# Kernel tuning notes

Hardware: AMD Instinct MI355X
Metric: run time of the kernel (lower is better)

## Reference

```python
import jax, jax.numpy as jnp
import numpy as np
import math

# Dims: d_model=192, expand=2 -> d_inner=d_ssm=384, headdim=64 -> nheads=6,
# d_state=128, K=4 scan directions, ngroups=1 (directions fused into state dim).
D_MODEL = 192
D_STATE = 128
D_CONV = 3
EXPAND = 2
HEADDIM = 64
CHUNK = 256
D_INNER = EXPAND * D_MODEL          # 384
D_SSM = D_INNER                     # default d_ssm (d_mlp == 0)
NHEADS = D_SSM // HEADDIM           # 6
K = 4                               # scan directions
HTOT = K * NHEADS                   # 24 heads in the fused scan
NSTATE = K * D_STATE                # 512 fused state dim (ngroups=1)
CONV_BC = 2 * D_STATE + NHEADS      # 262
B, H, W = 2, 64, 64


def _dwconv(x, w, b):
    # x: (B,C,H,W), w: (C,1,k,k) depthwise, SAME padding ((k-1)//2)
    y = jax.lax.conv_general_dilated(
        x, w, (1, 1), [(1, 1), (1, 1)],
        feature_group_count=x.shape[1],
        dimension_numbers=('NCHW', 'OIHW', 'NCHW'))
    return y + b[None, :, None, None]


def _ssd(x, dt_raw, A_logs, Bm, Cm, Ds, dt_bias):
    # Mamba2 chunked selective scan (dt_softplus=True, default dt_limit).
    # x: (b,l,h,p)  dt_raw: (b,l,h)  Bm,Cm: (b,l,n) with ngroups=1
    A = -jnp.exp(A_logs)                              # (h,)
    dt = jax.nn.softplus(dt_raw + dt_bias)            # (b,l,h)
    b, l, h, p = x.shape
    n = Bm.shape[-1]
    nc = l // CHUNK
    xc = x.reshape(b, nc, CHUNK, h, p)
    dtc = dt.reshape(b, nc, CHUNK, h)
    Bc = Bm.reshape(b, nc, CHUNK, n)
    Cc = Cm.reshape(b, nc, CHUNK, n)
    dA = dtc * A                                      # (b,nc,cs,h)
    acum = jnp.cumsum(dA, axis=2)
    # intra-chunk (causal, attention-like)
    a_t = jnp.transpose(acum, (0, 1, 3, 2))           # (b,nc,h,cs)
    diff = a_t[..., :, None] - a_t[..., None, :]      # (b,nc,h,i,j)
    causal = jnp.tril(jnp.ones((CHUNK, CHUNK), bool))
    Lmat = jnp.where(causal, jnp.exp(diff), 0.0)
    CB = jnp.einsum('bcin,bcjn->bcij', Cc, Bc)        # (b,nc,i,j)
    M = CB[:, :, None] * Lmat * jnp.transpose(dtc, (0, 1, 3, 2))[:, :, :, None, :]
    y = jnp.einsum('bchij,bcjhp->bcihp', M, xc)
    # chunk-final states
    decay_end = jnp.exp(acum[:, :, -1:, :] - acum)    # (b,nc,cs,h)
    states = jnp.einsum('bcjh,bcjn,bcjhp->bchpn', decay_end * dtc, Bc, xc)
    chunk_decay = jnp.exp(acum[:, :, -1, :])          # (b,nc,h)

    def step(S, inp):
        st, dec = inp
        return S * dec[:, :, None, None] + st, S

    S0 = jnp.zeros((b, h, p, n), x.dtype)
    _, prev = jax.lax.scan(step, S0, (jnp.moveaxis(states, 1, 0),
                                      jnp.moveaxis(chunk_decay, 1, 0)))
    prev = jnp.moveaxis(prev, 0, 1)                   # (b,nc,h,p,n)
    y = y + jnp.einsum('bcih,bcin,bchpn->bcihp', jnp.exp(acum), Cc, prev)
    y = y + xc * Ds[:, None]                          # D skip connection
    return y.reshape(b, l, h, p)


def _branch(u, u_cross, W_skip, W_xs, W_bcdt, conv_xs_w, conv_xs_b,
            conv_bc_w, conv_bc_b, dt_bias, A_logs, Ds, norm_w, W_out):
    Bb, Hh, Ww, _ = u.shape
    L = Hh * Ww
    z = (u @ W_skip).reshape(Bb, L, D_SSM)            # gate (d_mlp == 0)
    xs = jnp.transpose(u @ W_xs, (0, 3, 1, 2))        # (B,d_ssm,H,W)
    xs = jax.nn.silu(_dwconv(xs, conv_xs_w, conv_xs_b))
    bc = jnp.transpose(u_cross @ W_bcdt, (0, 3, 1, 2))
    bc = jax.nn.silu(_dwconv(bc, conv_bc_w, conv_bc_b))
    xbc = jnp.concatenate([xs, bc], axis=1)           # (B,646,H,W)
    C = xbc.shape[1]
    v = xbc.reshape(Bb, C, L)                         # HW raster
    vt = jnp.transpose(xbc, (0, 1, 3, 2)).reshape(Bb, C, L)  # WH raster
    hw = jnp.stack([v, vt], axis=1)                   # (B,2,C,L)
    xbcdt = jnp.concatenate([hw, jnp.flip(hw, axis=-1)], axis=1)  # (B,4,C,L)
    xp = xbcdt[:, :, :D_SSM]
    Bp = xbcdt[:, :, D_SSM:D_SSM + D_STATE]
    Cp = xbcdt[:, :, D_SSM + D_STATE:D_SSM + 2 * D_STATE]
    dtp = xbcdt[:, :, D_SSM + 2 * D_STATE:]
    x = xp.reshape(Bb, K * D_SSM, L).transpose(0, 2, 1).reshape(Bb, L, HTOT, HEADDIM)
    Bm = Bp.reshape(Bb, NSTATE, L).transpose(0, 2, 1)
    Cm = Cp.reshape(Bb, NSTATE, L).transpose(0, 2, 1)
    dt = dtp.reshape(Bb, HTOT, L).transpose(0, 2, 1)
    y = _ssd(x, dt, A_logs, Bm, Cm, Ds, dt_bias)      # (B,L,24,64)
    y = y.reshape(Bb, L, K, D_SSM)
    out_y = y[:, :, 0]
    inv_y = jnp.flip(y[:, :, 2:4], axis=1)            # (B,L,2,d_ssm)
    wh_y = y[:, :, 1].reshape(Bb, Ww, Hh, D_SSM).transpose(0, 2, 1, 3).reshape(Bb, L, D_SSM)
    invwh_y = inv_y[:, :, 1].reshape(Bb, Ww, Hh, D_SSM).transpose(0, 2, 1, 3).reshape(Bb, L, D_SSM)
    yf = out_y + inv_y[:, :, 0] + wh_y + invwh_y
    # gated RMSNorm (norm_before_gate=False, group_size == d_ssm)
    g = yf * jax.nn.silu(z)
    g = g * jax.lax.rsqrt(jnp.mean(g * g, axis=-1, keepdims=True) + 1e-5) * norm_w
    return (g @ W_out).reshape(Bb, Hh, Ww, D_MODEL)


def setup_inputs():
    key = jax.random.key(0)
    ks = jax.random.split(key, 16)
    f = lambda i, s: jax.random.normal(ks[i], s, jnp.float32)
    sc = 0.02
    dt = jnp.exp(jax.random.uniform(ks[10], (NHEADS,)) *
                 (math.log(0.1) - math.log(0.001)) + math.log(0.001))
    dt = jnp.maximum(dt, 1e-4)
    inv_dt = dt + jnp.log(-jnp.expm1(-dt))
    A = jax.random.uniform(ks[11], (NHEADS,), minval=1.0, maxval=16.0)
    return {
        'u1': f(0, (B, H, W, D_MODEL)),
        'u2': f(1, (B, H, W, D_MODEL)),
        'u2_cat_u1': f(2, (B, H, W, D_MODEL)),
        'u1_cat_u2': f(3, (B, H, W, D_MODEL)),
        'W_skip': f(4, (D_MODEL, D_SSM)) * sc,
        'W_xs': f(5, (D_MODEL, D_SSM)) * sc,
        'W_bcdt': f(6, (D_MODEL, CONV_BC)) * sc,
        'conv_xs_w': f(7, (D_SSM, 1, D_CONV, D_CONV)) * sc,
        'conv_xs_b': jnp.zeros((D_SSM,), jnp.float32),
        'conv_bc_w': f(8, (CONV_BC, 1, D_CONV, D_CONV)) * sc,
        'conv_bc_b': jnp.zeros((CONV_BC,), jnp.float32),
        'dt_bias': jnp.tile(inv_dt, K),
        'A_logs': jnp.tile(jnp.log(A), K),
        'Ds': jnp.ones((HTOT,), jnp.float32),
        'norm_w': jnp.ones((D_SSM,), jnp.float32),
        'W_out': f(9, (D_SSM, D_MODEL)) * sc,
    }


def reference(u1, u2, u2_cat_u1, u1_cat_u2, W_skip, W_xs, W_bcdt,
              conv_xs_w, conv_xs_b, conv_bc_w, conv_bc_b,
              dt_bias, A_logs, Ds, norm_w, W_out):
    args = (W_skip, W_xs, W_bcdt, conv_xs_w, conv_xs_b, conv_bc_w,
            conv_bc_b, dt_bias, A_logs, Ds, norm_w, W_out)
    out1 = _branch(u1, u2_cat_u1, *args)
    out2 = _branch(u2, u1_cat_u2, *args)
    return out1, out2
```

## Files before the change

kernel.cpp:

```cpp
#include <hip/hip_runtime.h>
#include <hip/hip_bf16.h>

#define DEV __device__ __forceinline__

static constexpr int LL   = 4096;
static constexpr int GG   = 4;
static constexpr int CBC  = 262;

typedef float f32x4  __attribute__((ext_vector_type(4)));
typedef short bf16x8 __attribute__((ext_vector_type(8)));
typedef short bf16x4v __attribute__((ext_vector_type(4)));
typedef short bf16x2 __attribute__((ext_vector_type(2)));

DEV int map_l(int s, int k) {
    int m = (k & 2) ? (4095 - s) : s;
    if (k & 1) m = ((m & 63) << 6) | (m >> 6);
    return m;
}
DEV float silu_f(float x) { return x / (1.f + __expf(-x)); }
DEV short f2bf(float f) {
    union { __hip_bfloat16 h; short s; } u;
    u.h = __float2bfloat16(f);
    return u.s;
}
DEV float bf2f(short s) {
    return __uint_as_float(((unsigned)(unsigned short)s) << 16);
}
DEV bf16x8 pack8(float4 a, float4 b) {
    bf16x8 r;
    r[0]=f2bf(a.x); r[1]=f2bf(a.y); r[2]=f2bf(a.z); r[3]=f2bf(a.w);
    r[4]=f2bf(b.x); r[5]=f2bf(b.y); r[6]=f2bf(b.z); r[7]=f2bf(b.w);
    return r;
}
DEV bf16x8 load8u(const __hip_bfloat16* p) {
    bf16x4v lo = *(const bf16x4v*)p;
    bf16x4v hi = *(const bf16x4v*)(p + 4);
    bf16x8 r;
    r[0]=lo[0]; r[1]=lo[1]; r[2]=lo[2]; r[3]=lo[3];
    r[4]=hi[0]; r[5]=hi[1]; r[6]=hi[2]; r[7]=hi[3];
    return r;
}
DEV void store16(__hip_bfloat16* p, const float* v) {
    bf16x8 a, b;
    #pragma unroll
    for (int e = 0; e < 8; ++e) { a[e] = f2bf(v[e]); b[e] = f2bf(v[8+e]); }
    *(bf16x8*)p = a;
    *((bf16x8*)p + 1) = b;
}
DEV void storeT(float v, float* p) { *p = v; }
DEV void storeT(float v, __hip_bfloat16* p) { *p = __float2bfloat16(v); }

__global__ void sentinel_k(float* out) { out[0] = 1e30f; }

__global__ void wt_all_k(const float* __restrict__ W_skip, const float* __restrict__ W_xs,
                         const float* __restrict__ W_bcdt, const float* __restrict__ W_out,
                         const float* __restrict__ norm_w, __hip_bfloat16* __restrict__ Wt)
{
    int idx = blockIdx.x * 256 + threadIdx.x;
    if (idx < 73728) {
        int n = idx / 192, k = idx - n * 192;
        Wt[idx] = __float2bfloat16(W_skip[(size_t)k * 384 + n]);
    } else if (idx < 147456) {
        int r = idx - 73728;
        int n = r / 192, k = r - n * 192;
        Wt[idx] = __float2bfloat16(W_xs[(size_t)k * 384 + n]);
    } else if (idx < 208896) {
        int r = idx - 147456;
        int n = r / 192, k = r - n * 192;
        Wt[idx] = __float2bfloat16(n < 262 ? W_bcdt[(size_t)k * 262 + n] : 0.f);
    } else if (idx < 282624) {
        int r = idx - 208896;
        int n = r / 384, k = r - n * 384;
        Wt[idx] = __float2bfloat16(W_out[(size_t)k * 192 + n] * norm_w[k]);
    }
}

template<int MODE, typename AT, typename OutT>
DEV void mgemm_body(const AT* __restrict__ A0, const AT* __restrict__ A1,
                    const __hip_bfloat16* __restrict__ Wt, OutT* __restrict__ C,
                    OutT* __restrict__ C2, int N, int Kd, int i0, int j0)
{
    int t = threadIdx.x;
    int w = t >> 6, lane = t & 63;
    int lr = lane & 15, kq = lane >> 4;
    const AT* arow[2];
    #pragma unroll
    for (int a = 0; a < 2; ++a) {
        int grow = i0 + w * 32 + a * 16 + lr;
        const AT* Ap = (grow < 8192) ? A0 : A1;
        arow[a] = Ap + (size_t)(grow & 8191) * Kd;
    }
    f32x4 acc[2][4] = {};
    for (int k0 = 0; k0 < Kd; k0 += 32) {
        int kb = k0 + kq * 8;
        bf16x8 af[2];
        #pragma unroll
        for (int a = 0; a < 2; ++a) {
            if constexpr (sizeof(AT) == 4)
                af[a] = pack8(*(const float4*)(arow[a] + kb), *(const float4*)(arow[a] + kb + 4));
            else
                af[a] = *(const bf16x8*)(arow[a] + kb);
        }
        #pragma unroll
        for (int b = 0; b < 4; ++b) {
            int n = j0 + b * 16 + lr;
            bf16x8 bfr = *(const bf16x8*)(Wt + (size_t)n * Kd + kb);
            #pragma unroll
            for (int a = 0; a < 2; ++a)
                acc[a][b] = __builtin_amdgcn_mfma_f32_16x16x32_bf16(af[a], bfr, acc[a][b], 0, 0, 0);
        }
    }
    #pragma unroll
    for (int a = 0; a < 2; ++a)
        #pragma unroll
        for (int b = 0; b < 4; ++b)
            #pragma unroll
            for (int r = 0; r < 4; ++r) {
                int row = i0 + w * 32 + a * 16 + kq * 4 + r;
                int col = j0 + b * 16 + lr;
                float v = acc[a][b][r];
                if constexpr (MODE == 0) {
                    if (col < N) storeT(v, &C[(size_t)row * N + col]);
                } else if constexpr (MODE == 1) {
                    if (col < N) storeT(silu_f(v), &C[(size_t)row * N + col]);
                } else {
                    if (col < 384) storeT(silu_f(v), &C[(size_t)row * 384 + col]);
                    else           storeT(v, &C2[(size_t)row * 384 + col - 384]);
                }
            }
}

template<int MODE, typename AT, typename OutT>
__global__ __launch_bounds__(256) void mgemm_k(
    const AT* __restrict__ A0, const AT* __restrict__ A1,
    const __hip_bfloat16* __restrict__ Wt, OutT* __restrict__ C,
    OutT* __restrict__ C2, int N, int Kd)
{
    mgemm_body<MODE, AT, OutT>(A0, A1, Wt, C, C2, N, Kd,
                               blockIdx.y * 128, blockIdx.x * 64);
}

__global__ __launch_bounds__(256) void mgemm_in_k(
    const float* __restrict__ u1, const float* __restrict__ u2,
    const float* __restrict__ u21, const float* __restrict__ u12,
    const __hip_bfloat16* __restrict__ Wt_skip, const __hip_bfloat16* __restrict__ Wt_bcdt,
    __hip_bfloat16* __restrict__ z_silu, __hip_bfloat16* __restrict__ pre_xs,
    __hip_bfloat16* __restrict__ pre_bc)
{
    int bid = blockIdx.x;
    if (bid < 1536) {
        mgemm_body<2, float, __hip_bfloat16>(u1, u2, Wt_skip, z_silu, pre_xs,
                                             768, 192, (bid / 12) * 128, (bid % 12) * 64);
    } else {
        int b = bid - 1536;
        mgemm_body<0, float, __hip_bfloat16>(u21, u12, Wt_bcdt, pre_bc, nullptr,
                                             CBC, 192, (b / 5) * 128, (b % 5) * 64);
    }
}

template<int STRIDE>
DEV void conv16(const __hip_bfloat16* __restrict__ pre, const float* __restrict__ cw,
                const float* __restrict__ cbia, int g, int h0, int w0, int chb,
                float* smem, float (*wsm)[9], float* bsm, int t)
{
    if (t < 144) wsm[t / 9][t % 9] = cw[(chb + t / 9) * 9 + t % 9];
    if (t < 16)  bsm[t] = cbia[chb + t];
    for (int i = t; i < 18 * 18 * 8; i += 256) {
        int cp = i & 7;
        int hw = i >> 3;
        int ww2 = hw % 18, hh = hw / 18;
        int gh = h0 - 1 + hh, gw = w0 - 1 + ww2;
        float v0 = 0.f, v1 = 0.f;
        if ((unsigned)gh < 64u && (unsigned)gw < 64u) {
            bf16x2 pv = *(const bf16x2*)(pre + ((size_t)g * LL + gh * 64 + gw) * STRIDE + chb + cp * 2);
            v0 = bf2f(pv[0]); v1 = bf2f(pv[1]);
        }
        smem[(hh * 18 + ww2) * 17 + cp * 2]     = v0;
        smem[(hh * 18 + ww2) * 17 + cp * 2 + 1] = v1;
    }
    __syncthreads();
    int h = t >> 4, w2 = t & 15;
    float out[16];
    #pragma unroll
    for (int ch = 0; ch < 16; ++ch) {
        float acc = bsm[ch];
        #pragma unroll
        for (int dy = 0; dy < 3; ++dy)
            #pragma unroll
            for (int dx = 0; dx < 3; ++dx)
                acc += smem[((h + dy) * 18 + (w2 + dx)) * 17 + ch] * wsm[ch][dy * 3 + dx];
        out[ch] = silu_f(acc);
    }
    __syncthreads();
    #pragma unroll
    for (int ch = 0; ch < 16; ++ch)
        smem[(h * 17 + w2) * 17 + ch] = out[ch];
    __syncthreads();
}

__global__ __launch_bounds__(256) void prep_k(
    const __hip_bfloat16* __restrict__ pre_bc, const float* __restrict__ cbw,
    const float* __restrict__ cbb, const __hip_bfloat16* __restrict__ pre_xs,
    const float* __restrict__ cxw, const float* __restrict__ cxb,
    const float* __restrict__ dt_bias, const float* __restrict__ A_logs,
    __hip_bfloat16* __restrict__ Bt, __hip_bfloat16* __restrict__ Cs,
    __hip_bfloat16* __restrict__ Bs, __hip_bfloat16* __restrict__ XtG,
    float* __restrict__ dt_arr, float* __restrict__ ac_arr,
    float* __restrict__ cdecay)
{
    __shared__ float smem[18 * 18 * 17];
    __shared__ float wsm[16][9];
    __shared__ float bsm[16];
    __shared__ float wsum[4];
    int bid = blockIdx.x;
    int t = threadIdx.x;
    if (bid < 2048) {
        int nt = bid & 31;
        int rest = bid >> 5;
        int wt = rest & 3, ht2 = (rest >> 2) & 3, g = rest >> 4;
        int h0 = ht2 * 16, w0 = wt * 16;
        int kd = nt >> 3, ch0 = (nt & 7) * 16;
        conv16<262>(pre_bc, cbw, cbb, g, h0, w0, ch0, smem, wsm, bsm, t);
        int pc = t >> 4, q = t & 15;
        int n = nt * 16 + pc;
        __hip_bfloat16* rowp = Bt + ((size_t)g * 512 + n) * 4096;
        float v[16];
        if (kd == 0) {
            #pragma unroll
            for (int e = 0; e < 16; ++e) v[e] = smem[(q * 17 + e) * 17 + pc];
            store16(rowp + (h0 + q) * 64 + w0, v);
        } else if (kd == 1) {
            #pragma unroll
            for (int e = 0; e < 16; ++e) v[e] = smem[(e * 17 + q) * 17 + pc];
            store16(rowp + (w0 + q) * 64 + h0, v);
        } else if (kd == 2) {
            #pragma unroll
            for (int e = 0; e < 16; ++e) v[e] = smem[(q * 17 + 15 - e) * 17 + pc];
            store16(rowp + 4095 - (h0 + q) * 64 - w0 - 15, v);
        } else {
            #pragma unroll
            for (int e = 0; e < 16; ++e) v[e] = smem[((15 - e) * 17 + q) * 17 + pc];
            store16(rowp + 4095 - (w0 + q) * 64 - h0 - 15, v);
        }
    } else if (bid < 4096) {
        int b2 = bid - 2048;
        int ct = b2 & 31;
        int rest = b2 >> 5;
        int wt = rest & 3, ht2 = (rest >> 2) & 3, g = rest >> 4;
        int h0 = ht2 * 16, w0 = wt * 16;
        bool isB = ct >= 16;
        int ctl = ct & 15;
        int kd = ctl >> 3, ch0 = (ctl & 7) * 16;
        int chb = (isB ? 0 : 128) + ch0;
        conv16<262>(pre_bc, cbw, cbb, g, h0, w0, chb, smem, wsm, bsm, t);
        __hip_bfloat16* dst = isB ? Bs : Cs;
        int h = t >> 4, w2 = t & 15;
        int s = (kd == 0) ? (h0 + h) * 64 + (w0 + w2) : (w0 + w2) * 64 + (h0 + h);
        float v[16];
        #pragma unroll
        for (int e = 0; e < 16; ++e) v[e] = smem[(h * 17 + w2) * 17 + e];
        store16(dst + ((size_t)g * 4096 + s) * 256 + kd * 128 + ch0, v);
    } else if (bid < 5632) {
        int b3 = bid - 4096;
        int ht = b3 % 24;
        int gc = b3 / 24;
        int c = gc & 15, g = gc >> 4;
        int k = ht / 6, h = ht % 6;
        int s = c * 256 + t;
        int l = map_l(s, k);
        int ch = 256 + h;
        float acc = cbb[ch];
        int hh0 = l >> 6, ww0 = l & 63;
        #pragma unroll
        for (int dy = 0; dy < 3; ++dy) {
            int gh = hh0 + dy - 1;
            if ((unsigned)gh >= 64u) continue;
            #pragma unroll
            for (int dx = 0; dx < 3; ++dx) {
                int gw = ww0 + dx - 1;
                if ((unsigned)gw >= 64u) continue;
                acc += __bfloat162float(pre_bc[((size_t)g * LL + gh * 64 + gw) * 262 + ch]) *
                       cbw[ch * 9 + dy * 3 + dx];
            }
        }
        float raw = silu_f(acc) + dt_bias[ht];
        float dtv = raw > 20.f ? raw : log1pf(__expf(raw));
        float dA = dtv * (-__expf(A_logs[ht]));
        float v = dA;
        #pragma unroll
        for (int off = 1; off < 64; off <<= 1) {
            float u = __shfl_up(v, off);
            if ((t & 63) >= off) v += u;
        }
        if ((t & 63) == 63) wsum[t >> 6] = v;
        __syncthreads();
        float add = 0.f;
        #pragma unroll
        for (int w2 = 0; w2 < 3; ++w2)
            if (w2 < (t >> 6)) add += wsum[w2];
        float cum = v + add;
        size_t base = ((size_t)g * 24 + ht) * LL + s;
        dt_arr[base] = dtv;
        ac_arr[base] = cum;
        if (t == 255) cdecay[(g * 24 + ht) * 16 + c] = __expf(cum);
    } else {
        int b4 = bid - 5632;
        int pct = b4 % 24;
        int rest = b4 / 24;
        int wt = rest & 3, ht2 = (rest >> 2) & 3, g = rest >> 4;
        int h0 = ht2 * 16, w0 = wt * 16, pc0 = pct * 16;
        conv16<384>(pre_xs, cxw, cxb, g, h0, w0, pc0, smem, wsm, bsm, t);
        int pc = t >> 4, q = t & 15;
        float v[16];
        size_t rowbase;
        #pragma unroll
        for (int e = 0; e < 16; ++e) v[e] = smem[(q * 17 + e) * 17 + pc];
        rowbase = ((size_t)(g * 2 + 0) * 384 + pc0 + pc) * 4096;
        store16(XtG + rowbase + (h0 + q) * 64 + w0, v);
        #pragma unroll
        for (int e = 0; e < 16; ++e) v[e] = smem[(e * 17 + q) * 17 + pc];
        rowbase = ((size_t)(g * 2 + 1) * 384 + pc0 + pc) * 4096;
        store16(XtG + rowbase + (w0 + q) * 64 + h0, v);
    }
}

__global__ __launch_bounds__(256) void cbst_k(
    const __hip_bfloat16* __restrict__ Cs, const __hip_bfloat16* __restrict__ Bs,
    __hip_bfloat16* __restrict__ CBm,
    const __hip_bfloat16* __restrict__ XtG, const __hip_bfloat16* __restrict__ Bt,
    const float* __restrict__ dt_arr, const float* __restrict__ ac_arr,
    __hip_bfloat16* __restrict__ states)
{
    __shared__ float wsh[256];
    __shared__ short xw[64][264];
    int bid = blockIdx.x;
    int t = threadIdx.x;
    int w = t >> 6, lane = t & 63;
    int lr = lane & 15, kq = lane >> 4;
    if (bid < 256) {
        int jq = bid & 3;
        int gc = bid >> 2;
        int c = gc & 15, g = gc >> 4;
        const __hip_bfloat16* cg = Cs + (size_t)g * 4096 * 256;
        const __hip_bfloat16* bsg = Bs + (size_t)g * 4096 * 256;
        f32x4 acc[4][4] = {};
        for (int ks = 0; ks < 16; ++ks) {
            int n0 = ks * 32 + kq * 8;
            int kd = n0 >> 7, nn = n0 & 127;
            int col = ((kd & 1) << 7) + nn;
            bf16x8 bfr[4];
            #pragma unroll
            for (int jt = 0; jt < 4; ++jt) {
                int j = jq * 64 + jt * 16 + lr;
                int s = c * 256 + j;
                int row = (kd < 2) ? s : 4095 - s;
                bfr[jt] = *(const bf16x8*)(bsg + (size_t)row * 256 + col);
            }
            #pragma unroll
            for (int iq = 0; iq < 4; ++iq) {
                int i = (w * 4 + iq) * 16 + lr;
                int s = c * 256 + i;
                int row = (kd < 2) ? s : 4095 - s;
                bf16x8 af = *(const bf16x8*)(cg + (size_t)row * 256 + col);
                #pragma unroll
                for (int jt = 0; jt < 4; ++jt)
                    acc[iq][jt] = __builtin_amdgcn_mfma_f32_16x16x32_bf16(af, bfr[jt], acc[iq][jt], 0, 0, 0);
            }
        }
        __hip_bfloat16* ob = CBm + (size_t)gc * 65536;
        #pragma unroll
        for (int iq = 0; iq < 4; ++iq)
            #pragma unroll
            for (int jt = 0; jt < 4; ++jt)
                #pragma unroll
                for (int r = 0; r < 4; ++r) {
                    int i = (w * 4 + iq) * 16 + kq * 4 + r;
                    int j = jq * 64 + jt * 16 + lr;
                    ob[(size_t)i * 256 + j] = __float2bfloat16(acc[iq][jt][r]);
                }
        return;
    }
    int sb = bid - 256;
    int task = (sb & 7) * 384 + (sb >> 3);
    int ht = task % 24;
    int rest = task / 24;
    int nh = rest & 1;
    int gc = rest >> 1;
    int c = gc & 15, g = gc >> 4;
    int kd = ht / 6;
    bool rev = kd >= 2;
    int c0 = (ht % 6) * 64;
    int n0 = nh * 256;
    const float* dtp = dt_arr + ((size_t)g * 24 + ht) * LL + c * 256;
    const float* acp = ac_arr + ((size_t)g * 24 + ht) * LL + c * 256;
    float ac_last = acp[255];
    wsh[t] = __expf(ac_last - acp[t]) * dtp[t];
    __syncthreads();
    const __hip_bfloat16* xg = XtG + ((size_t)(g * 2 + (kd & 1)) * 384 + c0) * 4096;
    #pragma unroll
    for (int r8 = 0; r8 < 8; ++r8) {
        int id = t + 256 * r8;
        int p = id >> 5;
        int jc = (id & 31) * 8;
        bf16x8 xv;
        if (!rev) {
            xv = *(const bf16x8*)(xg + (size_t)p * 4096 + c * 256 + jc);
        } else {
            bf16x8 tmp = load8u(xg + (size_t)p * 4096 + 4088 - c * 256 - jc);
            #pragma unroll
            for (int e = 0; e < 8; ++e) xv[e] = tmp[7 - e];
        }
        bf16x8 o;
        #pragma unroll
        for (int e = 0; e < 8; ++e) o[e] = f2bf(bf2f(xv[e]) * wsh[jc + e]);
        *(bf16x8*)&xw[p][jc] = o;
    }
    __syncthreads();
    const __hip_bfloat16* btg = Bt + ((size_t)g * 512 + n0) * 4096;
    f32x4 acc[4][4] = {};
    for (int ks = 0; ks < 8; ++ks) {
        int j0 = ks * 32 + kq * 8;
        bf16x8 af[4];
        #pragma unroll
        for (int pt = 0; pt < 4; ++pt)
            af[pt] = *(const bf16x8*)&xw[pt * 16 + lr][j0];
        #pragma unroll
        for (int nt = 0; nt < 4; ++nt) {
            int nl = (w * 4 + nt) * 16 + lr;
            bf16x8 bv = *(const bf16x8*)(btg + (size_t)nl * 4096 + c * 256 + j0);
            #pragma unroll
            for (int pt = 0; pt < 4; ++pt)
                acc[pt][nt] = __builtin_amdgcn_mfma_f32_16x16x32_bf16(af[pt], bv, acc[pt][nt], 0, 0, 0);
        }
    }
    __hip_bfloat16* ob = states + ((size_t)gc * 24 + ht) * 32768 + n0;
    #pragma unroll
    for (int pt = 0; pt < 4; ++pt)
        #pragma unroll
        for (int nt = 0; nt < 4; ++nt)
            #pragma unroll
            for (int r = 0; r < 4; ++r) {
                int p = pt * 16 + kq * 4 + r;
                int nl = (w * 4 + nt) * 16 + lr;
                ob[(size_t)p * 512 + nl] = __float2bfloat16(acc[pt][nt][r]);
            }
}

__global__ void scan_k(__hip_bfloat16* __restrict__ states, const float* __restrict__ cdecay)
{
    int idx = blockIdx.x * 256 + threadIdx.x;
    int g = idx / 98304;
    int r = idx - g * 98304;
    int ht = r >> 12;
    int pn8 = (r & 4095) * 8;
    const float* cd = cdecay + (g * 24 + ht) * 16;
    __hip_bfloat16* base = states + ((size_t)g * 384 + ht) * 32768 + pn8;
    float S[8] = {};
    #pragma unroll
    for (int c2 = 0; c2 < 16; ++c2) {
        bf16x8* p = (bf16x8*)(base + (size_t)c2 * 786432);
        bf16x8 tmp = *p;
        bf16x8 o;
        float dec = cd[c2];
        #pragma unroll
        for (int e = 0; e < 8; ++e) {
            o[e] = f2bf(S[e]);
            S[e] = S[e] * dec + bf2f(tmp[e]);
        }
        *p = o;
    }
}

__global__ __launch_bounds__(256) void yk(
    const __hip_bfloat16* __restrict__ XtG, const __hip_bfloat16* __restrict__ Cs,
    const __hip_bfloat16* __restrict__ CBm, const __hip_bfloat16* __restrict__ prev,
    const float* __restrict__ dt_arr, const float* __restrict__ ac_arr,
    const float* __restrict__ Ds, __hip_bfloat16* __restrict__ y4)
{
    __shared__ float acs[256], dts[256], ejdt[256];
    __shared__ short xl[64][264];
    int task = (blockIdx.x & 7) * 192 + (blockIdx.x >> 3);
    int ht = task % 24;
    int gc = task / 24;
    int c = gc & 15, g = gc >> 4;
    int kd = ht / 6;
    bool rev = kd >= 2;
    int c0 = (ht % 6) * 64;
    int t = threadIdx.x;
    int w = t >> 6, lane = t & 63;
    int lr = lane & 15, kq = lane >> 4;
    size_t abase = ((size_t)g * 24 + ht) * LL + c * 256;
    float ac_own = ac_arr[abase + t];
    float dt_own = dt_arr[abase + t];
    acs[t] = ac_own;
    dts[t] = dt_own;
    float acb0 = __shfl(ac_own, (t & 63) & ~31);
    ejdt[t] = __expf(acb0 - ac_own) * dt_own;
    const __hip_bfloat16* xg = XtG + ((size_t)(g * 2 + (kd & 1)) * 384 + c0) * 4096;
    #pragma unroll
    for (int r8 = 0; r8 < 8; ++r8) {
        int id = t + 256 * r8;
        int p = id >> 5;
        int jc = (id & 31) * 8;
        bf16x8 xv;
        if (!rev) {
            xv = *(const bf16x8*)(xg + (size_t)p * 4096 + c * 256 + jc);
        } else {
            bf16x8 tmp = load8u(xg + (size_t)p * 4096 + 4088 - c * 256 - jc);
            #pragma unroll
            for (int e = 0; e < 8; ++e) xv[e] = tmp[7 - e];
        }
        *(bf16x8*)&xl[p][jc] = xv;
    }
    __syncthreads();
    const __hip_bfloat16* cbb = CBm + (size_t)gc * 65536;
    const __hip_bfloat16* cg = Cs + (size_t)g * 4096 * 256;
    f32x4 acc[4][4] = {};
    const __hip_bfloat16* pv = prev + ((size_t)gc * 24 + ht) * 32768;
    auto ld2 = [&](int ns, bf16x8* afq, bf16x8* pb) {
        int n0 = ns * 32 + kq * 8;
        int kd2 = n0 >> 7, nn = n0 & 127;
        int col = ((kd2 & 1) << 7) + nn;
        #pragma unroll
        for (int q = 0; q < 4; ++q) {
            int i = (w + 4 * q) * 16 + lr;
            int s = c * 256 + i;
            int row = (kd2 < 2) ? s : 4095 - s;
            afq[q] = *(const bf16x8*)(cg + (size_t)row * 256 + col);
        }
        #pragma unroll
        for (int pt = 0; pt < 4; ++pt)
            pb[pt] = *(const bf16x8*)(pv + (size_t)(pt * 16 + lr) * 512 + n0);
    };
    auto fma2 = [&](bf16x8* afq, bf16x8* pb) {
        #pragma unroll
        for (int q = 0; q < 4; ++q)
            #pragma unroll
            for (int pt = 0; pt < 4; ++pt)
                acc[q][pt] = __builtin_amdgcn_mfma_f32_16x16x32_bf16(afq[q], pb[pt], acc[q][pt], 0, 0, 0);
    };
    {
        bf16x8 afA[4], pbA[4], afB[4], pbB[4];
        ld2(0, afA, pbA);
        #pragma unroll
        for (int ns = 0; ns < 16; ns += 2) {
            if (ns + 1 < 16) ld2(ns + 1, afB, pbB);
            fma2(afA, pbA);
            if (ns + 2 < 16) ld2(ns + 2, afA, pbA);
            fma2(afB, pbB);
        }
    }
    #pragma unroll
    for (int q = 0; q < 4; ++q)
        #pragma unroll
        for (int r = 0; r < 4; ++r) {
            float er = __expf(acs[(w + 4 * q) * 16 + kq * 4 + r]);
            #pragma unroll
            for (int pt = 0; pt < 4; ++pt) acc[q][pt][r] *= er;
        }
    float aci_q[4];
    #pragma unroll
    for (int q = 0; q < 4; ++q) aci_q[q] = acs[(w + 4 * q) * 16 + lr];
    for (int ks = 0; ks < 8; ++ks) {
        int j0 = ks * 32 + kq * 8;
        bf16x8 xb[4];
        #pragma unroll
        for (int pt = 0; pt < 4; ++pt)
            xb[pt] = *(const bf16x8*)&xl[pt * 16 + lr][j0];
        float acb = acs[ks * 32];
        float ej[8];
        #pragma unroll
        for (int e = 0; e < 8; ++e) ej[e] = ejdt[j0 + e];
        #pragma unroll
        for (int q = 0; q < 4; ++q) {
            int rt = w + 4 * q;
            if (rt < 2 * ks) continue;
            int i = rt * 16 + lr;
            float r2 = __expf(aci_q[q] - acb);
            bf16x8 cb8 = *(const bf16x8*)(cbb + (size_t)i * 256 + j0);
            bf16x8 af;
            if (rt >= 2 * ks + 2) {
                #pragma unroll
                for (int e = 0; e < 8; ++e)
                    af[e] = f2bf(r2 * ej[e] * bf2f(cb8[e]));
            } else {
                #pragma unroll
                for (int e = 0; e < 8; ++e) {
                    float coef = r2 * ej[e] * bf2f(cb8[e]);
                    af[e] = (j0 + e <= i) ? f2bf(coef) : (short)0;
                }
            }
            #pragma unroll
            for (int pt = 0; pt < 4; ++pt)
                acc[q][pt] = __builtin_amdgcn_mfma_f32_16x16x32_bf16(af, xb[pt], acc[q][pt], 0, 0, 0);
        }
    }
    float Dsv = Ds[ht];
    __hip_bfloat16* yb = y4 + (((size_t)(g * 4 + kd) * 4096 + c * 256) * 384) + c0;
    #pragma unroll
    for (int q = 0; q < 4; ++q) {
        int rt = w + 4 * q;
        #pragma unroll
        for (int pt = 0; pt < 4; ++pt) {
            int p = pt * 16 + lr;
            int ibase = rt * 16 + kq * 4;
            bf16x4v x4 = *(const bf16x4v*)&xl[p][ibase];
            #pragma unroll
            for (int r = 0; r < 4; ++r) {
                int i = ibase + r;
                float xv = bf2f(x4[r]);
                yb[(size_t)i * 384 + p] = __float2bfloat16(acc[q][pt][r] + Dsv * xv);
            }
        }
    }
}

__global__ __launch_bounds__(128) void gate_k(
    const __hip_bfloat16* __restrict__ y4, const __hip_bfloat16* __restrict__ z_silu,
    __hip_bfloat16* __restrict__ gn)
{
    int g = blockIdx.x >> 12;
    int l = blockIdx.x & 4095;
    int t = threadIdx.x;
    int Tl = ((l & 63) << 6) | (l >> 6);
    const __hip_bfloat16* p0 = y4 + ((size_t)(g * 4 + 0) * 4096 + l) * 384;
    const __hip_bfloat16* p1 = y4 + ((size_t)(g * 4 + 1) * 4096 + Tl) * 384;
    const __hip_bfloat16* p2 = y4 + ((size_t)(g * 4 + 2) * 4096 + 4095 - l) * 384;
    const __hip_bfloat16* p3 = y4 + ((size_t)(g * 4 + 3) * 4096 + 4095 - Tl) * 384;
    const __hip_bfloat16* zp = z_silu + ((size_t)g * LL + l) * 384;
    float gc[3]; float ssq = 0.f;
    #pragma unroll
    for (int q = 0; q < 3; ++q) {
        int cdim = t + 128 * q;
        float yf = __bfloat162float(p0[cdim]) + __bfloat162float(p1[cdim]) +
                   __bfloat162float(p2[cdim]) + __bfloat162float(p3[cdim]);
        float v = yf * __bfloat162float(zp[cdim]);
        gc[q] = v;
        ssq += v * v;
    }
    float v = ssq;
    #pragma unroll
    for (int off = 32; off > 0; off >>= 1) v += __shfl_down(v, off);
    __shared__ float tot[2];
    if ((t & 63) == 0) tot[t >> 6] = v;
    __syncthreads();
    float rs = rsqrtf((tot[0] + tot[1]) * (1.f / 384.f) + 1e-5f);
    __hip_bfloat16* gp = gn + ((size_t)g * LL + l) * 384;
    #pragma unroll
    for (int q = 0; q < 3; ++q) {
        int cdim = t + 128 * q;
        gp[cdim] = __float2bfloat16(gc[q] * rs);
    }
}

extern "C" void kernel_launch(void* const* d_in, const int* in_sizes, int n_in,
                              void* d_out, int out_size, void* d_ws, size_t ws_size,
                              hipStream_t stream)
{
    const float* u1      = (const float*)d_in[0];
    const float* u2      = (const float*)d_in[1];
    const float* u21     = (const float*)d_in[2];
    const float* u12     = (const float*)d_in[3];
    const float* W_skip  = (const float*)d_in[4];
    const float* W_xs    = (const float*)d_in[5];
    const float* W_bcdt  = (const float*)d_in[6];
    const float* cxw     = (const float*)d_in[7];
    const float* cxb     = (const float*)d_in[8];
    const float* cbw     = (const float*)d_in[9];
    const float* cbb     = (const float*)d_in[10];
    const float* dt_bias = (const float*)d_in[11];
    const float* A_logs  = (const float*)d_in[12];
    const float* Ds      = (const float*)d_in[13];
    const float* norm_w  = (const float*)d_in[14];
    const float* W_out   = (const float*)d_in[15];
    float* out = (float*)d_out;

    char* w = (char*)d_ws;
    size_t o_y4  = 0;
    size_t o_st  = o_y4 + 50331648;
    size_t o_z   = o_st + 100663296;
    size_t o_xtg = o_z  + 12582912;
    size_t o_bt  = o_xtg + 25165824;
    size_t o_cs  = o_bt + 16777216;
    size_t o_cbm = o_cs + 8388608;
    size_t o_dt  = o_cbm + 8388608;
    size_t o_ac  = o_dt + 1572864;
    size_t o_cd  = o_ac + 1572864;
    size_t o_wt  = o_cd + 8192;
    size_t o_bs  = o_wt + 589824;
    size_t total = o_bs + 8388608;
    if (total > ws_size) {
        sentinel_k<<<1, 1, 0, stream>>>(out);
        return;
    }
    __hip_bfloat16* y4     = (__hip_bfloat16*)(w + o_y4);
    __hip_bfloat16* states = (__hip_bfloat16*)(w + o_st);
    __hip_bfloat16* z_silu = (__hip_bfloat16*)(w + o_z);
    __hip_bfloat16* XtG    = (__hip_bfloat16*)(w + o_xtg);
    __hip_bfloat16* Bt     = (__hip_bfloat16*)(w + o_bt);
    __hip_bfloat16* Cs     = (__hip_bfloat16*)(w + o_cs);
    __hip_bfloat16* CBm    = (__hip_bfloat16*)(w + o_cbm);
    float*          dt_arr = (float*)(w + o_dt);
    float*          ac_arr = (float*)(w + o_ac);
    float*          cdecay = (float*)(w + o_cd);
    __hip_bfloat16* Wt     = (__hip_bfloat16*)(w + o_wt);
    __hip_bfloat16* Bs     = (__hip_bfloat16*)(w + o_bs);
    __hip_bfloat16* Wt_skip = Wt;
    __hip_bfloat16* Wt_bcdt = Wt + 147456;
    __hip_bfloat16* Wt_out  = Wt + 208896;
    __hip_bfloat16* pre_bc = (__hip_bfloat16*)(w + o_st);
    __hip_bfloat16* pre_xs = (__hip_bfloat16*)(w + o_st + 8650752);
    __hip_bfloat16* gn     = (__hip_bfloat16*)(w + o_st);

    dim3 blk(256);
    wt_all_k<<<dim3(1104), blk, 0, stream>>>(W_skip, W_xs, W_bcdt, W_out, norm_w, Wt);
    mgemm_in_k<<<dim3(2176), blk, 0, stream>>>(u1, u2, u21, u12, Wt_skip, Wt_bcdt,
                                               z_silu, pre_xs, pre_bc);
    prep_k<<<dim3(7168), blk, 0, stream>>>(pre_bc, cbw, cbb, pre_xs, cxw, cxb,
                                           dt_bias, A_logs, Bt, Cs, Bs, XtG,
                                           dt_arr, ac_arr, cdecay);
    cbst_k<<<dim3(3328), blk, 0, stream>>>(Cs, Bs, CBm, XtG, Bt, dt_arr, ac_arr, states);
    scan_k<<<dim3(1536), blk, 0, stream>>>(states, cdecay);
    yk<<<dim3(1536), blk, 0, stream>>>(XtG, Cs, CBm, states, dt_arr, ac_arr, Ds, y4);
    gate_k<<<dim3(16384), dim3(128), 0, stream>>>(y4, z_silu, gn);
    mgemm_k<0, __hip_bfloat16, float><<<dim3(3, 128), blk, 0, stream>>>(
        gn, gn + (size_t)8192 * 384, Wt_out, out, nullptr, 192, 384);
}
```

Measured before the change: 403.4 us.

## Fuse gated RMSNorm with output projection GEMM in one kernel

After: 408.1 us. Within noise of the previous version (+1.2%).

```diff
diff --git a/kernel.cpp b/kernel.cpp
--- a/kernel.cpp
+++ b/kernel.cpp
@@ -128,16 +128,6 @@
                     else           storeT(v, &C2[(size_t)row * 384 + col - 384]);
                 }
             }
-}
-
-template<int MODE, typename AT, typename OutT>
-__global__ __launch_bounds__(256) void mgemm_k(
-    const AT* __restrict__ A0, const AT* __restrict__ A1,
-    const __hip_bfloat16* __restrict__ Wt, OutT* __restrict__ C,
-    OutT* __restrict__ C2, int N, int Kd)
-{
-    mgemm_body<MODE, AT, OutT>(A0, A1, Wt, C, C2, N, Kd,
-                               blockIdx.y * 128, blockIdx.x * 64);
 }
 
 __global__ __launch_bounds__(256) void mgemm_in_k(
@@ -615,42 +605,83 @@
     }
 }
 
-__global__ __launch_bounds__(128) void gate_k(
+__global__ __launch_bounds__(256) void gateout_k(
     const __hip_bfloat16* __restrict__ y4, const __hip_bfloat16* __restrict__ z_silu,
-    __hip_bfloat16* __restrict__ gn)
-{
-    int g = blockIdx.x >> 12;
-    int l = blockIdx.x & 4095;
+    const __hip_bfloat16* __restrict__ Wt_out, float* __restrict__ out)
+{
+    __shared__ short gnl[64][392];
+    int b = blockIdx.x;
     int t = threadIdx.x;
-    int Tl = ((l & 63) << 6) | (l >> 6);
-    const __hip_bfloat16* p0 = y4 + ((size_t)(g * 4 + 0) * 4096 + l) * 384;
-    const __hip_bfloat16* p1 = y4 + ((size_t)(g * 4 + 1) * 4096 + Tl) * 384;
-    const __hip_bfloat16* p2 = y4 + ((size_t)(g * 4 + 2) * 4096 + 4095 - l) * 384;
-    const __hip_bfloat16* p3 = y4 + ((size_t)(g * 4 + 3) * 4096 + 4095 - Tl) * 384;
-    const __hip_bfloat16* zp = z_silu + ((size_t)g * LL + l) * 384;
-    float gc[3]; float ssq = 0.f;
-    #pragma unroll
-    for (int q = 0; q < 3; ++q) {
-        int cdim = t + 128 * q;
-        float yf = __bfloat162float(p0[cdim]) + __bfloat162float(p1[cdim]) +
-                   __bfloat162float(p2[cdim]) + __bfloat162float(p3[cdim]);
-        float v = yf * __bfloat162float(zp[cdim]);
-        gc[q] = v;
-        ssq += v * v;
-    }
-    float v = ssq;
-    #pragma unroll
-    for (int off = 32; off > 0; off >>= 1) v += __shfl_down(v, off);
-    __shared__ float tot[2];
-    if ((t & 63) == 0) tot[t >> 6] = v;
+    int row0 = b * 64;
+    {
+        int rloc = t >> 2, part = t & 3;
+        int row = row0 + rloc;
+        int g = row >> 12, l = row & 4095;
+        int Tl = ((l & 63) << 6) | (l >> 6);
+        const __hip_bfloat16* p0 = y4 + ((size_t)(g * 4 + 0) * 4096 + l) * 384;
+        const __hip_bfloat16* p1 = y4 + ((size_t)(g * 4 + 1) * 4096 + Tl) * 384;
+        const __hip_bfloat16* p2 = y4 + ((size_t)(g * 4 + 2) * 4096 + 4095 - l) * 384;
+        const __hip_bfloat16* p3 = y4 + ((size_t)(g * 4 + 3) * 4096 + 4095 - Tl) * 384;
+        const __hip_bfloat16* zp = z_silu + ((size_t)g * LL + l) * 384;
+        int cb = part * 96;
+        float vf[96];
+        float ssq = 0.f;
+        #pragma unroll
+        for (int cg = 0; cg < 12; ++cg) {
+            int cc = cb + cg * 8;
+            bf16x8 a0 = *(const bf16x8*)(p0 + cc);
+            bf16x8 a1 = *(const bf16x8*)(p1 + cc);
+            bf16x8 a2 = *(const bf16x8*)(p2 + cc);
+            bf16x8 a3 = *(const bf16x8*)(p3 + cc);
+            bf16x8 zv = *(const bf16x8*)(zp + cc);
+            #pragma unroll
+            for (int e = 0; e < 8; ++e) {
+                float yf = bf2f(a0[e]) + bf2f(a1[e]) + bf2f(a2[e]) + bf2f(a3[e]);
+                float v = yf * bf2f(zv[e]);
+                vf[cg * 8 + e] = v;
+                ssq += v * v;
+            }
+        }
+        ssq += __shfl_xor(ssq, 1);
+        ssq += __shfl_xor(ssq, 2);
+        float rs = rsqrtf(ssq * (1.f / 384.f) + 1e-5f);
+        #pragma unroll
+        for (int cg = 0; cg < 12; ++cg) {
+            bf16x8 o;
+            #pragma unroll
+            for (int e = 0; e < 8; ++e) o[e] = f2bf(vf[cg * 8 + e] * rs);
+            *(bf16x8*)&gnl[rloc][cb + cg * 8] = o;
+        }
+    }
     __syncthreads();
-    float rs = rsqrtf((tot[0] + tot[1]) * (1.f / 384.f) + 1e-5f);
-    __hip_bfloat16* gp = gn + ((size_t)g * LL + l) * 384;
-    #pragma unroll
-    for (int q = 0; q < 3; ++q) {
-        int cdim = t + 128 * q;
-        gp[cdim] = __float2bfloat16(gc[q] * rs);
-    }
+    int w = t >> 6, lane = t & 63;
+    int lr = lane & 15, kq = lane >> 4;
+    f32x4 acc[4][3] = {};
+    for (int k0 = 0; k0 < 384; k0 += 32) {
+        int kb = k0 + kq * 8;
+        bf16x8 af[4];
+        #pragma unroll
+        for (int a = 0; a < 4; ++a)
+            af[a] = *(const bf16x8*)&gnl[a * 16 + lr][kb];
+        #pragma unroll
+        for (int b2 = 0; b2 < 3; ++b2) {
+            int n = w * 48 + b2 * 16 + lr;
+            bf16x8 bfr = *(const bf16x8*)(Wt_out + (size_t)n * 384 + kb);
+            #pragma unroll
+            for (int a = 0; a < 4; ++a)
+                acc[a][b2] = __builtin_amdgcn_mfma_f32_16x16x32_bf16(af[a], bfr, acc[a][b2], 0, 0, 0);
+        }
+    }
+    #pragma unroll
+    for (int a = 0; a < 4; ++a)
+        #pragma unroll
+        for (int b2 = 0; b2 < 3; ++b2)
+            #pragma unroll
+            for (int r = 0; r < 4; ++r) {
+                int row = row0 + a * 16 + kq * 4 + r;
+                int col = w * 48 + b2 * 16 + lr;
+                out[(size_t)row * 192 + col] = acc[a][b2][r];
+            }
 }
 
 extern "C" void kernel_launch(void* const* d_in, const int* in_sizes, int n_in,
@@ -710,7 +741,6 @@
     __hip_bfloat16* Wt_out  = Wt + 208896;
     __hip_bfloat16* pre_bc = (__hip_bfloat16*)(w + o_st);
     __hip_bfloat16* pre_xs = (__hip_bfloat16*)(w + o_st + 8650752);
-    __hip_bfloat16* gn     = (__hip_bfloat16*)(w + o_st);
 
     dim3 blk(256);
     wt_all_k<<<dim3(1104), blk, 0, stream>>>(W_skip, W_xs, W_bcdt, W_out, norm_w, Wt);
@@ -722,7 +752,5 @@
     cbst_k<<<dim3(3328), blk, 0, stream>>>(Cs, Bs, CBm, XtG, Bt, dt_arr, ac_arr, states);
     scan_k<<<dim3(1536), blk, 0, stream>>>(states, cdecay);
     yk<<<dim3(1536), blk, 0, stream>>>(XtG, Cs, CBm, states, dt_arr, ac_arr, Ds, y4);
-    gate_k<<<dim3(16384), dim3(128), 0, stream>>>(y4, z_silu, gn);
-    mgemm_k<0, __hip_bfloat16, float><<<dim3(3, 128), blk, 0, stream>>>(
-        gn, gn + (size_t)8192 * 384, Wt_out, out, nullptr, 192, 384);
-}
+    gateout_k<<<dim3(256), blk, 0, stream>>>(y4, z_silu, Wt_out, out);
+}
```
